# Kernel optimization log

Hardware: AMD Instinct MI355X
Metric: run time of the kernel (lower is better)

## Reference

```python
import jax, jax.numpy as jnp
import numpy as np

C = 256
B, H, W = 2, 64, 64


def conv1x1(x, Wt, b):
    # x: [B, Cin, H, W], Wt: [Cout, Cin], b: [Cout]
    return jnp.einsum('bchw,oc->bohw', x, Wt) + b[None, :, None, None]


def setup_inputs() -> dict:
    key = jax.random.key(0)
    ks = jax.random.split(key, 16)
    s = 0.02
    d = {
        'input1': jax.random.normal(ks[0], (B, C, H, W), jnp.float32),
        'input2': jax.random.normal(ks[1], (B, C, H, W), jnp.float32),
        'Wq1': jax.random.normal(ks[2], (C // 4, C), jnp.float32) * s,
        'bq1': jnp.zeros((C // 4,), jnp.float32),
        'Wk1': jax.random.normal(ks[3], (C // 2, C), jnp.float32) * s,
        'bk1': jnp.zeros((C // 2,), jnp.float32),
        'Wv1': jax.random.normal(ks[4], (C, C), jnp.float32) * s,
        'bv1': jnp.zeros((C,), jnp.float32),
        'Wq2': jax.random.normal(ks[5], (C // 4, C), jnp.float32) * s,
        'bq2': jnp.zeros((C // 4,), jnp.float32),
        'Wk2': jax.random.normal(ks[6], (C // 2, C), jnp.float32) * s,
        'bk2': jnp.zeros((C // 2,), jnp.float32),
        'Wv2': jax.random.normal(ks[7], (C, C), jnp.float32) * s,
        'bv2': jnp.zeros((C,), jnp.float32),
        'gamma': jax.random.normal(ks[8], (1,), jnp.float32) * 0.1,
    }
    return d


def reference(input1, input2, Wq1, bq1, Wk1, bk1, Wv1, bv1,
              Wq2, bq2, Wk2, bk2, Wv2, bv2, gamma):
    b, c, h, w = input1.shape
    hw = h * w
    q1 = conv1x1(input1, Wq1, bq1)                      # [B, C/4, H, W]
    k1 = conv1x1(input1, Wk1, bk1).reshape(b, -1, hw)   # [B, C/2, HW]
    v1 = conv1x1(input1, Wv1, bv1).reshape(b, -1, hw)   # [B, C,   HW]
    q2 = conv1x1(input2, Wq2, bq2)
    k2 = conv1x1(input2, Wk2, bk2).reshape(b, -1, hw)
    v2 = conv1x1(input2, Wv2, bv2).reshape(b, -1, hw)

    # cat on new dim 2 then 'b c t h w -> b (c t) h w' interleaves q1/q2 channels
    q = jnp.stack([q1, q2], axis=2).reshape(b, c // 2, hw)  # [B, C/2, HW]
    q = q.transpose(0, 2, 1)                                # [B, HW, C/2]

    a1 = jax.nn.softmax(jnp.einsum('bnc,bcm->bnm', q, k1), axis=-1)  # [B, HW, HW]
    out1 = jnp.einsum('bcm,bnm->bcn', v1, a1).reshape(b, c, h, w)
    out1 = gamma[0] * out1 + input1

    a2 = jax.nn.softmax(jnp.einsum('bnc,bcm->bnm', q, k2), axis=-1)
    out2 = jnp.einsum('bcm,bnm->bcn', v2, a2).reshape(b, c, h, w)
    out2 = gamma[0] * out2 + input2
    return (out1, out2)
```

## Files before the change

kernel.cpp:

```cpp
#include <hip/hip_runtime.h>

typedef __attribute__((ext_vector_type(8)))  short bf16x8;
typedef __attribute__((ext_vector_type(4)))  float f32x4;
typedef __attribute__((ext_vector_type(16))) float f32x16;
typedef __attribute__((ext_vector_type(8)))  unsigned short u16x8;

#define HW 4096
#define CDIM 256

__device__ __forceinline__ unsigned short f2bf(float f) {
    union { float f; unsigned u; } v; v.f = f;
    unsigned r = v.u + 0x7fffu + ((v.u >> 16) & 1u);
    return (unsigned short)(r >> 16);
}
__device__ __forceinline__ unsigned short truncbf(float f) {
    union { float f; unsigned u; } v; v.f = f;
    return (unsigned short)(v.u >> 16);
}
__device__ __forceinline__ float bf2f(unsigned short u) {
    union { unsigned u; float f; } v; v.u = ((unsigned)u) << 16;
    return v.f;
}
__device__ __forceinline__ unsigned pk2(float hi, float lo) {
    union { float f; unsigned u; } a, b; a.f = hi; b.f = lo;
    return __builtin_amdgcn_perm(a.u, b.u, 0x07060302u);
}
__device__ __forceinline__ void gl_lds16(const void* g, void* l) {
    __builtin_amdgcn_global_load_lds(
        (const __attribute__((address_space(1))) unsigned int*)(unsigned long long)g,
        (__attribute__((address_space(3))) unsigned int*)(unsigned int)(unsigned long long)l,
        16, 0, 0);
}

__global__ __launch_bounds__(256) void wpack_kernel(
    const float* __restrict__ Wq1, const float* __restrict__ Wk1,
    const float* __restrict__ Wv1, const float* __restrict__ Wq2,
    const float* __restrict__ Wk2, const float* __restrict__ Wv2,
    unsigned short* __restrict__ Wpk)
{
    const int i  = blockIdx.x * 256 + threadIdx.x;
    const int c4 = i & 63;
    const int r6 = i >> 6;
    const int inp = r6 / 448;
    const int o   = r6 - inp * 448;
    const float* src;
    int orow;
    if (o < 64)       { src = inp ? Wq2 : Wq1; orow = o; }
    else if (o < 192) { src = inp ? Wk2 : Wk1; orow = o - 64; }
    else              { src = inp ? Wv2 : Wv1; orow = o - 192; }
    const float4 v = *(const float4*)(src + (size_t)orow * CDIM + c4 * 4);
    uint2 pkd; pkd.x = pk2(v.y, v.x); pkd.y = pk2(v.w, v.z);
    ((uint2*)Wpk)[i] = pkd;
}

__global__ __launch_bounds__(256) void proj_kernel(
    const float* __restrict__ in1, const float* __restrict__ in2,
    const float* __restrict__ bq1, const float* __restrict__ bk1,
    const float* __restrict__ bv1, const float* __restrict__ bq2,
    const float* __restrict__ bk2, const float* __restrict__ bv2,
    const unsigned short* __restrict__ Wpk,
    unsigned short* __restrict__ Qg, unsigned short* __restrict__ Kg,
    unsigned short* __restrict__ Vg)
{
    __shared__ unsigned xb[32 * 128];

    const int bid   = blockIdx.x;
    const int ntile = bid & 127;
    const int inp   = (bid >> 7) & 1;
    const int b     = bid >> 8;

    const float* X  = (inp ? in2 : in1) + (size_t)b * CDIM * HW;
    const float* bq = inp ? bq2 : bq1;
    const float* bk = inp ? bk2 : bk1;
    const float* bv = inp ? bv2 : bv1;
    const unsigned short* Wb = Wpk + (size_t)inp * 448 * CDIM;

    const int tid  = threadIdx.x;
    const int lane = tid & 63;
    const int w    = tid >> 6;
    const int l15  = lane & 15, quad = lane >> 4;
    const int n0   = ntile * 32;

#pragma unroll
    for (int t = 0; t < 4; ++t) {
        const int idx = t * 256 + tid;
        const int cp  = idx >> 3;
        const int n4  = idx & 7;
        const float* p0 = X + (size_t)(cp * 2) * HW + n0 + n4 * 4;
        const float4 a = *(const float4*)p0;
        const float4 bb = *(const float4*)(p0 + HW);
        const float av[4] = {a.x, a.y, a.z, a.w};
        const float bv4[4] = {bb.x, bb.y, bb.z, bb.w};
#pragma unroll
        for (int r = 0; r < 4; ++r) {
            const int n = n4 * 4 + r;
            xb[n * 128 + (((cp >> 2) ^ (n & 7)) << 2) + (cp & 3)] = pk2(bv4[r], av[r]);
        }
    }
    __syncthreads();

    f32x4 acc[7][2];
#pragma unroll
    for (int i = 0; i < 7; ++i)
#pragma unroll
        for (int j = 0; j < 2; ++j) acc[i][j] = (f32x4){0.f, 0.f, 0.f, 0.f};

#pragma unroll
    for (int kk = 0; kk < 8; ++kk) {
        bf16x8 xf[2];
#pragma unroll
        for (int ns = 0; ns < 2; ++ns) {
            const int nrow = ns * 16 + l15;
            xf[ns] = *(const bf16x8*)&xb[nrow * 128 + (((kk * 4 + quad) ^ (nrow & 7)) << 2)];
        }
#pragma unroll
        for (int os = 0; os < 7; ++os) {
            const int ob = w * 7 + os;
            const int og = ob * 16 + l15;
            const bf16x8 wf = *(const bf16x8*)(Wb + (size_t)og * CDIM + kk * 32 + quad * 8);
            if (ob < 12) {
#pragma unroll
                for (int ns = 0; ns < 2; ++ns)
                    acc[os][ns] = __builtin_amdgcn_mfma_f32_16x16x32_bf16(xf[ns], wf, acc[os][ns], 0, 0, 0);
            } else {
#pragma unroll
                for (int ns = 0; ns < 2; ++ns)
                    acc[os][ns] = __builtin_amdgcn_mfma_f32_16x16x32_bf16(wf, xf[ns], acc[os][ns], 0, 0, 0);
            }
        }
    }

    const size_t qbase = (size_t)b * HW * 128;
    const size_t kbase = (size_t)(b * 2 + inp) * HW * 128;
    const size_t vbase = (size_t)(b * 2 + inp) * (size_t)CDIM * HW;
#pragma unroll
    for (int os = 0; os < 7; ++os) {
        const int ob = w * 7 + os;
        if (ob < 4) {
            const int o = ob * 16 + l15;
            const float bb = bq[o];
#pragma unroll
            for (int ns = 0; ns < 2; ++ns) {
                const f32x4 d = acc[os][ns];
#pragma unroll
                for (int r = 0; r < 4; ++r) {
                    const int n = n0 + ns * 16 + quad * 4 + r;
                    Qg[qbase + (size_t)n * 128 + 2 * o + inp] = f2bf(d[r] + bb);
                }
            }
        } else if (ob < 12) {
            const int c = (ob - 4) * 16 + l15;
            const float bb = bk[c];
#pragma unroll
            for (int ns = 0; ns < 2; ++ns) {
                const f32x4 d = acc[os][ns];
#pragma unroll
                for (int r = 0; r < 4; ++r) {
                    const int n = n0 + ns * 16 + quad * 4 + r;
                    Kg[kbase + (size_t)n * 128 + c] = f2bf(d[r] + bb);
                }
            }
        } else {
            const int c0 = (ob - 12) * 16 + quad * 4;
#pragma unroll
            for (int ns = 0; ns < 2; ++ns) {
                const f32x4 d = acc[os][ns];
#pragma unroll
                for (int r = 0; r < 4; ++r) {
                    const int n = n0 + ns * 16 + l15;
                    Vg[vbase + (size_t)(c0 + r) * HW + n] = f2bf(d[r] + bv[c0 + r]);
                }
            }
        }
    }
}

__global__ __launch_bounds__(256) void attn_kernel(
    const unsigned short* __restrict__ Qg, const unsigned short* __restrict__ Kg,
    const unsigned short* __restrict__ Vg,
    unsigned short* __restrict__ Op, float* __restrict__ Lp)
{
    __shared__ unsigned short kbuf[2][32 * 16 * 8];
    __shared__ unsigned short vbuf[2][256 * 4 * 8];
    __shared__ unsigned short pbuf[4][32 * 40];
    __shared__ float lbuf[4][32];

    const int bid = blockIdx.x;
    const int set = (bid & 7) >> 1;
    const int att = set & 1, b = set >> 1;
    const int sub = ((bid >> 3) << 1) | (bid & 1);
    const int mh  = sub & 1, qt = sub >> 1;
    const int n0g = qt * 64;
    const int mbase = mh * 2048;
    const int tid = threadIdx.x;
    const int lane = tid & 63, w = tid >> 6;
    const int l31 = lane & 31, h = lane >> 5;
    const int ng = w >> 1, ch = w & 1;

    const unsigned short* Qb = Qg + (size_t)b * HW * 128;
    const unsigned short* Kb = Kg + (size_t)(b * 2 + att) * HW * 128;
    const unsigned short* Vb = Vg + (size_t)(b * 2 + att) * (size_t)CDIM * HW;

    bf16x8 aQ[8];
    {
        const int n = n0g + ng * 32 + l31;
#pragma unroll
        for (int kk = 0; kk < 8; ++kk)
            aQ[kk] = *(const bf16x8*)(Qb + (size_t)n * 128 + kk * 16 + h * 8);
    }

    f32x16 acc[4];
#pragma unroll
    for (int i = 0; i < 4; ++i)
#pragma unroll
        for (int r = 0; r < 16; ++r) acc[i][r] = 0.f;
    float lsum[16];
#pragma unroll
    for (int r = 0; r < 16; ++r) lsum[r] = 0.f;

    const unsigned short* ksrc[2]; unsigned short* kdst[2][2];
    const unsigned short* vsrc[4]; unsigned short* vdst[2][4];
#pragma unroll
    for (int t = 0; t < 2; ++t) {
        const int L = (t * 4 + w) * 64 + lane;
        const int ml = L >> 4, s = L & 15;
        const int g = s ^ (ml & 15);
        ksrc[t] = Kb + (size_t)ml * 128 + g * 8;
        kdst[0][t] = &kbuf[0][L * 8]; kdst[1][t] = &kbuf[1][L * 8];
    }
#pragma unroll
    for (int t = 0; t < 4; ++t) {
        const int L = (t * 4 + w) * 64 + lane;
        const int c = L >> 2, s = L & 3;
        const int g = s ^ ((c >> 2) & 3);
        vsrc[t] = Vb + (size_t)c * HW + g * 8;
        vdst[0][t] = &vbuf[0][L * 8]; vdst[1][t] = &vbuf[1][L * 8];
    }

    auto stage = [&](int mt, int bs) {
        const int m0 = mbase + mt * 32;
#pragma unroll
        for (int t = 0; t < 2; ++t) gl_lds16(ksrc[t] + (size_t)m0 * 128, kdst[bs][t]);
#pragma unroll
        for (int t = 0; t < 4; ++t) gl_lds16(vsrc[t] + m0, vdst[bs][t]);
    };

    stage(0, 0);

    unsigned short* pw = pbuf[w];

    for (int mt = 0; mt < 64; ++mt) {
        __syncthreads();
        if (mt + 1 < 64) stage(mt + 1, (mt + 1) & 1);
        const int cur = mt & 1;

        f32x16 sa, sb;
#pragma unroll
        for (int r = 0; r < 16; ++r) { sa[r] = 0.f; sb[r] = 0.f; }
#pragma unroll
        for (int kk = 0; kk < 4; ++kk) {
            bf16x8 bK = *(const bf16x8*)&kbuf[cur][(l31 * 16 + ((kk * 2 + h) ^ (l31 & 15))) * 8];
            sa = __builtin_amdgcn_mfma_f32_32x32x16_bf16(aQ[kk], bK, sa, 0, 0, 0);
        }
#pragma unroll
        for (int kk = 4; kk < 8; ++kk) {
            bf16x8 bK = *(const bf16x8*)&kbuf[cur][(l31 * 16 + ((kk * 2 + h) ^ (l31 & 15))) * 8];
            sb = __builtin_amdgcn_mfma_f32_32x32x16_bf16(aQ[kk], bK, sb, 0, 0, 0);
        }

#pragma unroll
        for (int r = 0; r < 16; ++r) {
            const float p = __expf(sa[r] + sb[r]);
            lsum[r] += p;
            pw[((r & 3) + 8 * (r >> 2) + 4 * h) * 40 + l31] = truncbf(p);
        }

        bf16x8 bP[2];
#pragma unroll
        for (int k2 = 0; k2 < 2; ++k2)
            bP[k2] = *(const bf16x8*)&pw[l31 * 40 + k2 * 16 + h * 8];
#pragma unroll
        for (int cf = 0; cf < 4; ++cf) {
            const int c = ch * 128 + cf * 32 + l31;
#pragma unroll
            for (int k2 = 0; k2 < 2; ++k2) {
                bf16x8 aV = *(const bf16x8*)&vbuf[cur][(c * 4 + ((k2 * 2 + h) ^ ((c >> 2) & 3))) * 8];
                acc[cf] = __builtin_amdgcn_mfma_f32_32x32x16_bf16(aV, bP[k2], acc[cf], 0, 0, 0);
            }
        }
    }

#pragma unroll
    for (int off = 1; off < 32; off <<= 1)
#pragma unroll
        for (int r = 0; r < 16; ++r) lsum[r] += __shfl_xor(lsum[r], off, 64);
    if (l31 == 0) {
#pragma unroll
        for (int r = 0; r < 16; ++r)
            lbuf[w][(r & 3) + 8 * (r >> 2) + 4 * h] = lsum[r];
    }

    const int nn = n0g + ng * 32 + l31;
    if (ch == 0) Lp[(size_t)(mh * 4 + set) * HW + nn] = lbuf[w][l31];

    const size_t obase = (size_t)(mh * 4 + set) * CDIM * HW;
#pragma unroll
    for (int cf = 0; cf < 4; ++cf) {
#pragma unroll
        for (int r = 0; r < 16; ++r) {
            const int c = ch * 128 + cf * 32 + (r & 3) + 8 * (r >> 2) + 4 * h;
            Op[obase + (size_t)c * HW + nn] = f2bf(acc[cf][r]);
        }
    }
}

__global__ __launch_bounds__(256) void combine_kernel(
    const unsigned short* __restrict__ Op, const float* __restrict__ Lp,
    const float* __restrict__ in1, const float* __restrict__ in2,
    const float* __restrict__ gamma_p, float* __restrict__ out)
{
    const size_t i8 = ((size_t)blockIdx.x * 256 + threadIdx.x) * 8;
    const int oset = (int)(i8 >> 20);
    const int att = oset >> 1, b = oset & 1;
    const int pset = b * 2 + att;
    const size_t rem = i8 & 1048575u;
    const int n = (int)(i8 & 4095);

    const u16x8 o0 = *(const u16x8*)(Op + ((size_t)pset << 20) + rem);
    const u16x8 o1 = *(const u16x8*)(Op + ((size_t)pset << 20) + rem + ((size_t)4 << 20));
    const f32x4 la0 = *(const f32x4*)(Lp + (size_t)pset * HW + n);
    const f32x4 la1 = *(const f32x4*)(Lp + (size_t)pset * HW + n + 4);
    const f32x4 lb0 = *(const f32x4*)(Lp + (size_t)(4 + pset) * HW + n);
    const f32x4 lb1 = *(const f32x4*)(Lp + (size_t)(4 + pset) * HW + n + 4);
    const float* inb = (att ? in2 : in1) + (size_t)b * CDIM * HW + rem;
    const float g = *gamma_p;

    const f32x4 iv0 = *(const f32x4*)(inb);
    const f32x4 iv1 = *(const f32x4*)(inb + 4);
    f32x4 r0, r1;
#pragma unroll
    for (int j = 0; j < 4; ++j) {
        const float ov = bf2f((unsigned short)o0[j]) + bf2f((unsigned short)o1[j]);
        r0[j] = g * ov / (la0[j] + lb0[j]) + iv0[j];
    }
#pragma unroll
    for (int j = 0; j < 4; ++j) {
        const float ov = bf2f((unsigned short)o0[j + 4]) + bf2f((unsigned short)o1[j + 4]);
        r1[j] = g * ov / (la1[j] + lb1[j]) + iv1[j];
    }
    *(f32x4*)(out + i8) = r0;
    *(f32x4*)(out + i8 + 4) = r1;
}

extern "C" void kernel_launch(void* const* d_in, const int* in_sizes, int n_in,
                              void* d_out, int out_size, void* d_ws, size_t ws_size,
                              hipStream_t stream) {
    const float* in1 = (const float*)d_in[0];
    const float* in2 = (const float*)d_in[1];
    const float* Wq1 = (const float*)d_in[2];  const float* bq1 = (const float*)d_in[3];
    const float* Wk1 = (const float*)d_in[4];  const float* bk1 = (const float*)d_in[5];
    const float* Wv1 = (const float*)d_in[6];  const float* bv1 = (const float*)d_in[7];
    const float* Wq2 = (const float*)d_in[8];  const float* bq2 = (const float*)d_in[9];
    const float* Wk2 = (const float*)d_in[10]; const float* bk2 = (const float*)d_in[11];
    const float* Wv2 = (const float*)d_in[12]; const float* bv2 = (const float*)d_in[13];
    const float* gamma = (const float*)d_in[14];

    unsigned short* Qg = (unsigned short*)d_ws;
    unsigned short* Kg = Qg + (size_t)2 * HW * 128;
    unsigned short* Vg = Kg + (size_t)4 * HW * 128;
    unsigned short* Op = Vg + (size_t)4 * CDIM * HW;
    float*          Lp = (float*)(Op + (size_t)8 * CDIM * HW);
    unsigned short* Wpk = Op;

    wpack_kernel<<<224, 256, 0, stream>>>(Wq1, Wk1, Wv1, Wq2, Wk2, Wv2, Wpk);
    proj_kernel<<<512, 256, 0, stream>>>(in1, in2, bq1, bk1, bv1, bq2, bk2, bv2,
                                         Wpk, Qg, Kg, Vg);
    attn_kernel<<<512, 256, 0, stream>>>(Qg, Kg, Vg, Op, Lp);
    combine_kernel<<<2048, 256, 0, stream>>>(Op, Lp, in1, in2, gamma, (float*)d_out);
}
```

Measured before the change: 218.4 us.

## Transpose score MFMA and use permlane32 swap to build P in registers

Swaps the operands of the QK^T MFMA so each lane holds scores for one query row. The P operand for the PV MFMA is then built with bf16 packing and permlane32_swap, which removes the per-wave LDS staging buffer and the cross-lane row-sum reduction. It also folds log2(e) into Q in the projection kernel, so the softmax can use a native exp2. P packing now truncates to bf16 via perm, as before, and the row sum collapses to a single shuffle.

```diff
diff --git a/kernel.cpp b/kernel.cpp
--- a/kernel.cpp
+++ b/kernel.cpp
@@ -8,14 +8,16 @@
 #define HW 4096
 #define CDIM 256
 
+#if __has_builtin(__builtin_amdgcn_exp2f)
+#define EXP2(x) __builtin_amdgcn_exp2f(x)
+#else
+#define EXP2(x) exp2f(x)
+#endif
+
 __device__ __forceinline__ unsigned short f2bf(float f) {
     union { float f; unsigned u; } v; v.f = f;
     unsigned r = v.u + 0x7fffu + ((v.u >> 16) & 1u);
     return (unsigned short)(r >> 16);
-}
-__device__ __forceinline__ unsigned short truncbf(float f) {
-    union { float f; unsigned u; } v; v.f = f;
-    return (unsigned short)(v.u >> 16);
 }
 __device__ __forceinline__ float bf2f(unsigned short u) {
     union { unsigned u; float f; } v; v.u = ((unsigned)u) << 16;
@@ -145,7 +147,8 @@
 #pragma unroll
                 for (int r = 0; r < 4; ++r) {
                     const int n = n0 + ns * 16 + quad * 4 + r;
-                    Qg[qbase + (size_t)n * 128 + 2 * o + inp] = f2bf(d[r] + bb);
+                    Qg[qbase + (size_t)n * 128 + 2 * o + inp] =
+                        f2bf((d[r] + bb) * 1.4426950408889634f);
                 }
             }
         } else if (ob < 12) {
@@ -182,8 +185,6 @@
 {
     __shared__ unsigned short kbuf[2][32 * 16 * 8];
     __shared__ unsigned short vbuf[2][256 * 4 * 8];
-    __shared__ unsigned short pbuf[4][32 * 40];
-    __shared__ float lbuf[4][32];
 
     const int bid = blockIdx.x;
     const int set = (bid & 7) >> 1;
@@ -214,9 +215,7 @@
     for (int i = 0; i < 4; ++i)
 #pragma unroll
         for (int r = 0; r < 16; ++r) acc[i][r] = 0.f;
-    float lsum[16];
-#pragma unroll
-    for (int r = 0; r < 16; ++r) lsum[r] = 0.f;
+    float lsum = 0.f;
 
     const unsigned short* ksrc[2]; unsigned short* kdst[2][2];
     const unsigned short* vsrc[4]; unsigned short* vdst[2][4];
@@ -247,8 +246,6 @@
 
     stage(0, 0);
 
-    unsigned short* pw = pbuf[w];
-
     for (int mt = 0; mt < 64; ++mt) {
         __syncthreads();
         if (mt + 1 < 64) stage(mt + 1, (mt + 1) & 1);
@@ -260,25 +257,39 @@
 #pragma unroll
         for (int kk = 0; kk < 4; ++kk) {
             bf16x8 bK = *(const bf16x8*)&kbuf[cur][(l31 * 16 + ((kk * 2 + h) ^ (l31 & 15))) * 8];
-            sa = __builtin_amdgcn_mfma_f32_32x32x16_bf16(aQ[kk], bK, sa, 0, 0, 0);
+            sa = __builtin_amdgcn_mfma_f32_32x32x16_bf16(bK, aQ[kk], sa, 0, 0, 0);
         }
 #pragma unroll
         for (int kk = 4; kk < 8; ++kk) {
             bf16x8 bK = *(const bf16x8*)&kbuf[cur][(l31 * 16 + ((kk * 2 + h) ^ (l31 & 15))) * 8];
-            sb = __builtin_amdgcn_mfma_f32_32x32x16_bf16(aQ[kk], bK, sb, 0, 0, 0);
-        }
-
+            sb = __builtin_amdgcn_mfma_f32_32x32x16_bf16(bK, aQ[kk], sb, 0, 0, 0);
+        }
+
+        float p[16];
 #pragma unroll
         for (int r = 0; r < 16; ++r) {
-            const float p = __expf(sa[r] + sb[r]);
-            lsum[r] += p;
-            pw[((r & 3) + 8 * (r >> 2) + 4 * h) * 40 + l31] = truncbf(p);
+            p[r] = EXP2(sa[r] + sb[r]);
+            lsum += p[r];
         }
 
         bf16x8 bP[2];
 #pragma unroll
-        for (int k2 = 0; k2 < 2; ++k2)
-            bP[k2] = *(const bf16x8*)&pw[l31 * 40 + k2 * 16 + h * 8];
+        for (int k2 = 0; k2 < 2; ++k2) {
+            const float* pp = p + k2 * 8;
+            const unsigned a0 = pk2(pp[1], pp[0]);
+            const unsigned a1 = pk2(pp[3], pp[2]);
+            const unsigned b0 = pk2(pp[5], pp[4]);
+            const unsigned b1 = pk2(pp[7], pp[6]);
+            auto s0 = __builtin_amdgcn_permlane32_swap(a0, b0, false, false);
+            auto s1 = __builtin_amdgcn_permlane32_swap(a1, b1, false, false);
+            union { unsigned u[4]; bf16x8 v; } uu;
+            uu.u[0] = s0[0];
+            uu.u[1] = s1[0];
+            uu.u[2] = s0[1];
+            uu.u[3] = s1[1];
+            bP[k2] = uu.v;
+        }
+
 #pragma unroll
         for (int cf = 0; cf < 4; ++cf) {
             const int c = ch * 128 + cf * 32 + l31;
@@ -290,18 +301,9 @@
         }
     }
 
-#pragma unroll
-    for (int off = 1; off < 32; off <<= 1)
-#pragma unroll
-        for (int r = 0; r < 16; ++r) lsum[r] += __shfl_xor(lsum[r], off, 64);
-    if (l31 == 0) {
-#pragma unroll
-        for (int r = 0; r < 16; ++r)
-            lbuf[w][(r & 3) + 8 * (r >> 2) + 4 * h] = lsum[r];
-    }
-
+    const float ltot = lsum + __shfl_xor(lsum, 32, 64);
     const int nn = n0g + ng * 32 + l31;
-    if (ch == 0) Lp[(size_t)(mh * 4 + set) * HW + nn] = lbuf[w][l31];
+    if (ch == 0 && h == 0) Lp[(size_t)(mh * 4 + set) * HW + nn] = ltot;
 
     const size_t obase = (size_t)(mh * 4 + set) * CDIM * HW;
 #pragma unroll
```

Result: faster. 209.6 us (-4.0%).
